# Optimization experiments

Measured on AMD Instinct MI355X. Metric: run time of the kernel, lower is better.

Reference implementation:

```python
import jax, jax.numpy as jnp
import numpy as np

N, E, G, F = 50000, 800000, 64, 128
R_MAX = 5.0
P_CUT = 6.0
NUM_BESSEL = 8


def sph_harm(u):
    # component-normalized real spherical harmonics up to l=3 on unit vectors u [E,3]
    x, y, z = u[:, 0], u[:, 1], u[:, 2]
    one = jnp.ones_like(x)
    s3, s5, s15 = np.sqrt(3.0), np.sqrt(5.0), np.sqrt(15.0)
    c1, c2, c3 = np.sqrt(35.0 / 8.0), np.sqrt(105.0), np.sqrt(21.0 / 8.0)
    c4, c5 = np.sqrt(7.0) / 2.0, np.sqrt(105.0) / 2.0
    x2, y2, z2 = x * x, y * y, z * z
    comps = [
        one,
        s3 * x, s3 * y, s3 * z,
        s15 * x * y, s15 * y * z, 0.5 * s5 * (3.0 * z2 - 1.0), s15 * x * z, 0.5 * s15 * (x2 - y2),
        c1 * y * (3.0 * x2 - y2), c2 * x * y * z, c3 * y * (5.0 * z2 - 1.0),
        c4 * z * (5.0 * z2 - 3.0), c3 * x * (5.0 * z2 - 1.0), c5 * z * (x2 - y2),
        c1 * x * (x2 - 3.0 * y2),
    ]
    return jnp.stack(comps, axis=-1)  # [E,16]


def radial_embedding(r):
    # Bessel basis with polynomial cutoff envelope; r [E]
    n = jnp.arange(1, NUM_BESSEL + 1, dtype=r.dtype)
    bessel = np.sqrt(2.0 / R_MAX) * jnp.sin(n * jnp.pi * r[:, None] / R_MAX) / r[:, None]
    u = r / R_MAX
    p = P_CUT
    env = (1.0 - (p + 1.0) * (p + 2.0) / 2.0 * u ** p
           + p * (p + 2.0) * u ** (p + 1.0)
           - p * (p + 1.0) / 2.0 * u ** (p + 2.0))
    env = env * (r < R_MAX).astype(r.dtype)
    return bessel * env[:, None]  # [E,8]


def setup_inputs() -> dict:
    key = jax.random.key(0)
    ks = jax.random.split(key, 12)
    return {
        "positions": jax.random.normal(ks[0], (N, 3), dtype=jnp.float32),
        "node_attrs": jax.random.uniform(ks[1], (N, 10), dtype=jnp.float32),
        "shifts": jnp.zeros((E, 3), dtype=jnp.float32),
        "edge_index": jax.random.randint(ks[2], (2, E), 0, N),
        "batch": jnp.sort(jax.random.randint(ks[3], (N,), 0, G)),
        "num_graphs": G,
        "W_emb": 0.1 * jax.random.normal(ks[4], (10, F), dtype=jnp.float32),
        "atomic_energies_t": jax.random.normal(ks[5], (10,), dtype=jnp.float32),
        "W_r": 0.1 * jax.random.normal(ks[6], (2, NUM_BESSEL, F), dtype=jnp.float32),
        "w_sh": 0.1 * jax.random.normal(ks[7], (2, 16), dtype=jnp.float32),
        "W_out": 0.1 * jax.random.normal(ks[8], (2, F, F), dtype=jnp.float32),
        "W_skip": 0.1 * jax.random.normal(ks[9], (2, 10, F), dtype=jnp.float32),
        "w_read": 0.1 * jax.random.normal(ks[10], (2, F), dtype=jnp.float32),
    }


def reference(positions, node_attrs, shifts, edge_index, batch, num_graphs,
              W_emb, atomic_energies_t, W_r, w_sh, W_out, W_skip, w_read):
    snd, rcv = edge_index[0], edge_index[1]

    def energy_fn(pos):
        vec = pos[rcv] - pos[snd] + shifts                      # [E,3] edge gather
        r = jnp.sqrt(jnp.sum(vec * vec, axis=-1) + 1e-12)       # [E]
        Y = sph_harm(vec / r[:, None])                          # [E,16]
        eb = radial_embedding(r)                                # [E,8]
        h = node_attrs @ W_emb                                  # [N,F] node embedding
        e0 = jax.ops.segment_sum(node_attrs @ atomic_energies_t, batch, num_segments=num_graphs)
        energy = e0
        for i in range(W_r.shape[0]):                           # interaction layers
            R = eb @ W_r[i]                                     # [E,F] radial weights
            s = Y @ w_sh[i]                                     # [E] angular weight
            m = h[snd] * R * s[:, None]                         # [E,F] messages
            agg = jax.ops.segment_sum(m, rcv, num_segments=pos.shape[0])  # [N,F]
            h = agg @ W_out[i] + node_attrs @ W_skip[i]
            node_e = h @ w_read[i]                              # [N] readout
            energy = energy + jax.ops.segment_sum(node_e, batch, num_segments=num_graphs)
        return energy                                           # [G]

    energy = energy_fn(positions)
    forces = -jax.grad(lambda p: energy_fn(p).sum())(positions)
    return energy, forces
```

## Files before the change

### kernel.cpp

```cpp
#include <hip/hip_runtime.h>

#define NN 50000
#define EE 800000
#define GG 64
#define FF 128
#define NBES 8
#define RECW 8
#define RMAXF 5.0f
#define PI_F 3.14159265358979323846f
#define NB ((NN + 255) / 256)

#define S3  1.7320508075688772f
#define S5  2.23606797749979f
#define S15 3.872983346207417f
#define C1c 2.091650066335189f
#define C2c 10.246950765959598f
#define C3c 1.62018517460196f
#define C4c 1.3228756555322954f
#define C5c 5.123475382979799f
#define CCB 0.6324555320336759f

__device__ __forceinline__ float shc_s(float x, float y, float z, const float* __restrict__ w) {
    float x2 = x * x, y2 = y * y, z2 = z * z;
    return w[0]
        + w[1] * (S3 * x) + w[2] * (S3 * y) + w[3] * (S3 * z)
        + w[4] * (S15 * x * y) + w[5] * (S15 * y * z) + w[6] * (0.5f * S5 * (3.f * z2 - 1.f))
        + w[7] * (S15 * x * z) + w[8] * (0.5f * S15 * (x2 - y2))
        + w[9] * (C1c * y * (3.f * x2 - y2)) + w[10] * (C2c * x * y * z)
        + w[11] * (C3c * y * (5.f * z2 - 1.f)) + w[12] * (C4c * z * (5.f * z2 - 3.f))
        + w[13] * (C3c * x * (5.f * z2 - 1.f)) + w[14] * (C5c * z * (x2 - y2))
        + w[15] * (C1c * x * (x2 - 3.f * y2));
}

__device__ __forceinline__ void shc_grad(float x, float y, float z, const float* __restrict__ w,
                                         float& gx, float& gy, float& gz) {
    float x2 = x * x, y2 = y * y, z2 = z * z;
    gx = w[1] * S3 + w[4] * (S15 * y) + w[7] * (S15 * z) + w[8] * (S15 * x)
       + w[9] * (6.f * C1c * x * y) + w[10] * (C2c * y * z) + w[13] * (C3c * (5.f * z2 - 1.f))
       + w[14] * (2.f * C5c * x * z) + w[15] * (3.f * C1c * (x2 - y2));
    gy = w[2] * S3 + w[4] * (S15 * x) + w[5] * (S15 * z) - w[8] * (S15 * y)
       + w[9] * (3.f * C1c * (x2 - y2)) + w[10] * (C2c * x * z) + w[11] * (C3c * (5.f * z2 - 1.f))
       - w[14] * (2.f * C5c * y * z) - w[15] * (6.f * C1c * x * y);
    gz = w[3] * S3 + w[5] * (S15 * y) + w[6] * (3.f * S5 * z) + w[7] * (S15 * x)
       + w[10] * (C2c * x * y) + w[11] * (10.f * C3c * y * z) + w[12] * (C4c * (15.f * z2 - 3.f))
       + w[13] * (10.f * C3c * x * z) + w[14] * (C5c * (x2 - y2));
}


__global__ __launch_bounds__(256) void count_kernel(const int* __restrict__ ei,
                                                    int* __restrict__ cnt,
                                                    int* __restrict__ rank_r,
                                                    int* __restrict__ rank_s) {
    int e = blockIdx.x * 256 + threadIdx.x;
    if (e >= EE) return;
    rank_r[e] = atomicAdd(&cnt[ei[EE + e]], 1);
    rank_s[e] = atomicAdd(&cnt[NN + ei[e]], 1);
}

__global__ __launch_bounds__(256) void scan_partial(const int* __restrict__ cnt,
                                                    int* __restrict__ parts) {
    __shared__ int wsum[4];
    int b = blockIdx.x;
    int half = b / NB;
    int cb = b - half * NB;
    int i = cb * 256 + threadIdx.x;
    int v = (i < NN) ? cnt[(size_t)half * NN + i] : 0;
    int x = v;
#pragma unroll
    for (int o = 32; o > 0; o >>= 1) x += __shfl_xor(x, o);
    int lane = threadIdx.x & 63, wid = threadIdx.x >> 6;
    if (lane == 0) wsum[wid] = x;
    __syncthreads();
    if (threadIdx.x == 0) parts[b] = wsum[0] + wsum[1] + wsum[2] + wsum[3];
}

__global__ __launch_bounds__(256) void scan_parts(int* __restrict__ parts,
                                                  int* __restrict__ off) {
    __shared__ int wsum[4];
    __shared__ int carry_s;
    int lane = threadIdx.x & 63, wid = threadIdx.x >> 6;
    for (int h = 0; h < 2; h++) {
        if (threadIdx.x == 0) carry_s = 0;
        __syncthreads();
        for (int base = 0; base < NB; base += 256) {
            int i = base + threadIdx.x;
            int v = (i < NB) ? parts[h * NB + i] : 0;
            int x = v;
#pragma unroll
            for (int d = 1; d < 64; d <<= 1) {
                int y = __shfl_up(x, d);
                if (lane >= d) x += y;
            }
            if (lane == 63) wsum[wid] = x;
            __syncthreads();
            int pre = 0;
#pragma unroll
            for (int w = 0; w < 4; w++) if (w < wid) pre += wsum[w];
            int total = wsum[0] + wsum[1] + wsum[2] + wsum[3];
            int carry = carry_s;
            if (i < NB) parts[h * NB + i] = carry + pre + x - v;
            __syncthreads();
            if (threadIdx.x == 0) carry_s = carry + total;
            __syncthreads();
        }
        if (threadIdx.x == 0) off[(size_t)h * (NN + 1) + NN] = carry_s;
        __syncthreads();
    }
}

__global__ __launch_bounds__(256) void scan_apply(const int* __restrict__ cnt,
                                                  const int* __restrict__ parts,
                                                  int* __restrict__ off) {
    __shared__ int wsum[4];
    int b = blockIdx.x;
    int half = b / NB;
    int cb = b - half * NB;
    int i = cb * 256 + threadIdx.x;
    int v = (i < NN) ? cnt[(size_t)half * NN + i] : 0;
    int lane = threadIdx.x & 63, wid = threadIdx.x >> 6;
    int x = v;
#pragma unroll
    for (int d = 1; d < 64; d <<= 1) {
        int y = __shfl_up(x, d);
        if (lane >= d) x += y;
    }
    if (lane == 63) wsum[wid] = x;
    __syncthreads();
    int pre = 0;
#pragma unroll
    for (int w = 0; w < 4; w++) if (w < wid) pre += wsum[w];
    if (i < NN) off[(size_t)half * (NN + 1) + i] = parts[b] + pre + x - v;
}

__global__ __launch_bounds__(256) void fill_kernel(const int* __restrict__ ei,
                                                   const int* __restrict__ off,
                                                   const int* __restrict__ rank_r,
                                                   const int* __restrict__ rank_s,
                                                   int* __restrict__ jr,
                                                   int* __restrict__ js,
                                                   int* __restrict__ psl_j) {
    int e = blockIdx.x * 256 + threadIdx.x;
    if (e >= EE) return;
    int snd = ei[e], rcv = ei[EE + e];
    int sr = off[rcv] + rank_r[e];
    int ss = off[(NN + 1) + snd] + rank_s[e];
    jr[e] = sr;
    js[e] = ss;
    psl_j[ss] = sr;
}


__global__ __launch_bounds__(256) void edge_geom(const float* __restrict__ pos,
                                                 const float* __restrict__ shifts,
                                                 const int* __restrict__ ei,
                                                 const float* __restrict__ wsh,
                                                 const int* __restrict__ jr,
                                                 const int* __restrict__ js,
                                                 float* __restrict__ rec,
                                                 float* __restrict__ ebs0,
                                                 float* __restrict__ ebs1) {
    int e = blockIdx.x * 256 + threadIdx.x;
    if (e >= EE) return;
    int snd = ei[e];
    int rcv = ei[EE + e];
    float vx = pos[rcv * 3 + 0] - pos[snd * 3 + 0] + shifts[e * 3 + 0];
    float vy = pos[rcv * 3 + 1] - pos[snd * 3 + 1] + shifts[e * 3 + 1];
    float vz = pos[rcv * 3 + 2] - pos[snd * 3 + 2] + shifts[e * 3 + 2];
    float r2 = vx * vx + vy * vy + vz * vz + 1e-12f;
    float r = sqrtf(r2);
    float inv_r = 1.0f / r;
    float x = vx * inv_r, y = vy * inv_r, z = vz * inv_r;

    float s0 = shc_s(x, y, z, wsh);
    float s1v = shc_s(x, y, z, wsh + 16);

    float* rc = rec + (size_t)jr[e] * RECW;
    *(float4*)&rc[0] = make_float4(x, y, z, inv_r);
    *(float4*)&rc[4] = make_float4(s0, s1v, __int_as_float(snd), __int_as_float(rcv));

    float u = r * (1.0f / RMAXF);
    float th = PI_F * u;
    float s1 = sinf(th), c1 = cosf(th);
    float u2 = u * u, u3 = u2 * u, u6 = u3 * u3, u7 = u6 * u, u8 = u6 * u2;
    float valid = (r < RMAXF) ? 1.f : 0.f;
    float env = (1.f - 28.f * u6 + 48.f * u7 - 21.f * u8) * valid;
    float base = CCB * inv_r * env;
    float ebv[NBES];
    {
        float sk = s1, skm = 0.f;
        float tc = 2.f * c1;
#pragma unroll
        for (int k = 0; k < NBES; k++) {
            ebv[k] = sk * base;
            float sn = tc * sk - skm; skm = sk; sk = sn;
        }
    }
    float* p0p = ebs0 + (size_t)jr[e] * 8;
    *(float4*)&p0p[0] = make_float4(ebv[0] * s0, ebv[1] * s0, ebv[2] * s0, ebv[3] * s0);
    *(float4*)&p0p[4] = make_float4(ebv[4] * s0, ebv[5] * s0, ebv[6] * s0, ebv[7] * s0);
    float* p1p = ebs1 + (size_t)js[e] * 8;
    *(float4*)&p1p[0] = make_float4(ebv[0] * s1v, ebv[1] * s1v, ebv[2] * s1v, ebv[3] * s1v);
    *(float4*)&p1p[4] = make_float4(ebv[4] * s1v, ebv[5] * s1v, ebv[6] * s1v, ebv[7] * s1v);
}


__global__ __launch_bounds__(256) void e1_csr(const float* __restrict__ ebs1,
                                              const int* __restrict__ off_snd,
                                              float* __restrict__ E1) {
    int gid = blockIdx.x * 256 + threadIdx.x;
    int n = gid >> 3;
    int k_l = gid & 7;
    if (n >= NN) return;
    int beg = off_snd[n], end = off_snd[n + 1];
    float acc = 0.f;
    for (int s = beg; s < end; s++) acc += ebs1[(size_t)s * 8 + k_l];
    E1[(size_t)n * 8 + k_l] = acc;
}


__global__ __launch_bounds__(128) void a1_kernel(const float* __restrict__ Wout1,
                                                 const float* __restrict__ wread1,
                                                 const float* __restrict__ Wskip1,
                                                 const float* __restrict__ ae,
                                                 float* __restrict__ a1,
                                                 float* __restrict__ askip) {
    int f = threadIdx.x;
    float s = 0.f;
    for (int k = 0; k < FF; k++) s += Wout1[f * FF + k] * wread1[k];
    a1[f] = s;
    if (f < 10) {
        float t = 0.f;
        for (int k = 0; k < FF; k++) t += Wskip1[f * FF + k] * wread1[k];
        askip[f] = t + ae[f];
    }
}

__global__ __launch_bounds__(128) void cd_kernel(const float* __restrict__ Wout0,
                                                 const float* __restrict__ wread0,
                                                 const float* __restrict__ a1,
                                                 const float* __restrict__ Wr1,
                                                 float* __restrict__ c0,
                                                 float* __restrict__ D) {
    int fp = threadIdx.x;
    float c = 0.f;
    float d[NBES];
#pragma unroll
    for (int k = 0; k < NBES; k++) d[k] = 0.f;
    for (int f = 0; f < FF; f++) {
        float w = Wout0[fp * FF + f];
        c += wread0[f] * w;
        float aw = a1[f] * w;
#pragma unroll
        for (int k = 0; k < NBES; k++) d[k] += aw * Wr1[k * FF + f];
    }
    c0[fp] = c;
#pragma unroll
    for (int k = 0; k < NBES; k++) D[k * FF + fp] = d[k];
}

__global__ __launch_bounds__(256) void gw_kernel(const float* __restrict__ W_emb,
                                                 const float* __restrict__ Wr0,
                                                 const float* __restrict__ Wout0,
                                                 float* __restrict__ GW) {
    int idx = blockIdx.x * 256 + threadIdx.x;
    if (idx >= 80 * FF) return;
    int fp = idx & 127;
    int p = idx >> 7;
    int a = p >> 3, k = p & 7;
    float s = 0.f;
    for (int f = 0; f < FF; f++)
        s += W_emb[a * FF + f] * Wr0[k * FF + f] * Wout0[f * FF + fp];
    GW[p * FF + fp] = s;
}

__global__ __launch_bounds__(256) void tmc_kernel(const float* __restrict__ D,
                                                  const float* __restrict__ c0,
                                                  const float* __restrict__ W_emb,
                                                  const float* __restrict__ Wr0,
                                                  float* __restrict__ T,
                                                  float* __restrict__ Mc) {
    for (int i = threadIdx.x; i < 720; i += 256) {
        if (i < 640) {
            int kp = i / 80;
            int p0 = i - kp * 80;
            int k = p0 / 10, a = p0 - k * 10;
            float s = 0.f;
            for (int f = 0; f < FF; f++)
                s += D[kp * FF + f] * W_emb[a * FF + f] * Wr0[k * FF + f];
            T[i] = s;
        } else {
            int p0 = i - 640;
            int k = p0 / 10, a = p0 - k * 10;
            float s = 0.f;
            for (int f = 0; f < FF; f++)
                s += c0[f] * W_emb[a * FF + f] * Wr0[k * FF + f];
            Mc[p0] = s;
        }
    }
}


#define P0_BLOCKS 2048
__global__ __launch_bounds__(256) void p0_kernel(const float* __restrict__ rec,
                                                 const float* __restrict__ ebs0,
                                                 const int* __restrict__ off,
                                                 const float* __restrict__ attrs,
                                                 float* __restrict__ P0) {
    int wv = (blockIdx.x * 256 + threadIdx.x) >> 6;
    int lane = threadIdx.x & 63;
    int nwaves = P0_BLOCKS * 4;
    int jsub = lane >> 3;
    int k_l = lane & 7;

    for (int n = wv; n < NN; n += nwaves) {
        int beg = off[n], end = off[n + 1];
        float acc[10];
#pragma unroll
        for (int a = 0; a < 10; a++) acc[a] = 0.f;
        for (int i = beg; i < end; i += 8) {
            int j = i + jsub;
            bool v = (j < end);
            int jc = v ? j : beg;
            float es = ebs0[(size_t)jc * 8 + k_l];
            if (!v) es = 0.f;
            int snd = __float_as_int(rec[(size_t)jc * RECW + 6]);
            const float* at = attrs + (size_t)snd * 10;
#pragma unroll
            for (int a = 0; a < 10; a++) acc[a] += at[a] * es;
        }
#pragma unroll
        for (int a = 0; a < 10; a++) {
            acc[a] += __shfl_xor(acc[a], 8);
            acc[a] += __shfl_xor(acc[a], 16);
            acc[a] += __shfl_xor(acc[a], 32);
        }
        if (jsub == 0) {
#pragma unroll
            for (int a = 0; a < 10; a++)
                P0[(size_t)n * 80 + a * 8 + k_l] = acc[a];
        }
    }
}


#define GEMM_BLOCKS 512
__global__ __launch_bounds__(256, 2) void h1_gemm(const float* __restrict__ P0,
                                                  const float* __restrict__ GW,
                                                  const float* __restrict__ attrs,
                                                  const float* __restrict__ Wskip,
                                                  const float* __restrict__ wread,
                                                  float* __restrict__ h1,
                                                  float* __restrict__ node_e) {
    __shared__ float sb[80][FF];
    __shared__ float sa[32][80];
    int t = threadIdx.x;
#pragma unroll
    for (int j = 0; j < 10; j++) {
        int flat4 = j * 256 + t;
        int row = flat4 >> 5;
        int col = (flat4 & 31) * 4;
        *(float4*)&sb[row][col] = *(const float4*)&GW[row * FF + col];
    }

    int g = t >> 5;
    int f0 = (t & 31) * 4;
    const int NTILES = (NN + 31) / 32;

    for (int tile = blockIdx.x; tile < NTILES; tile += GEMM_BLOCKS) {
        __syncthreads();
#pragma unroll
        for (int j = 0; j < 3; j++) {
            int flat4 = j * 256 + t;
            if (flat4 < 640) {
                int row = flat4 / 20;
                int col = (flat4 - row * 20) * 4;
                int n = tile * 32 + row;
                float4 v = make_float4(0.f, 0.f, 0.f, 0.f);
                if (n < NN) v = *(const float4*)&P0[(size_t)n * 80 + col];
                *(float4*)&sa[row][col] = v;
            }
        }
        __syncthreads();

        float acc[4][4];
#pragma unroll
        for (int i = 0; i < 4; i++)
#pragma unroll
            for (int j = 0; j < 4; j++) acc[i][j] = 0.f;

        for (int kk = 0; kk < 80; kk += 4) {
            float4 bv0 = *(const float4*)&sb[kk + 0][f0];
            float4 bv1 = *(const float4*)&sb[kk + 1][f0];
            float4 bv2 = *(const float4*)&sb[kk + 2][f0];
            float4 bv3 = *(const float4*)&sb[kk + 3][f0];
#pragma unroll
            for (int ni = 0; ni < 4; ni++) {
                float4 av = *(const float4*)&sa[g * 4 + ni][kk];
                acc[ni][0] += av.x * bv0.x + av.y * bv1.x + av.z * bv2.x + av.w * bv3.x;
                acc[ni][1] += av.x * bv0.y + av.y * bv1.y + av.z * bv2.y + av.w * bv3.y;
                acc[ni][2] += av.x * bv0.z + av.y * bv1.z + av.z * bv2.z + av.w * bv3.z;
                acc[ni][3] += av.x * bv0.w + av.y * bv1.w + av.z * bv2.w + av.w * bv3.w;
            }
        }

#pragma unroll
        for (int ni = 0; ni < 4; ni++) {
            int n = tile * 32 + g * 4 + ni;
            bool valid = (n < NN);
#pragma unroll
            for (int a = 0; a < 10; a++) {
                float att = valid ? attrs[n * 10 + a] : 0.f;
                float4 wk = *(const float4*)&Wskip[a * FF + f0];
                acc[ni][0] += att * wk.x;
                acc[ni][1] += att * wk.y;
                acc[ni][2] += att * wk.z;
                acc[ni][3] += att * wk.w;
            }
            if (valid) {
                float4 out;
                out.x = acc[ni][0]; out.y = acc[ni][1];
                out.z = acc[ni][2]; out.w = acc[ni][3];
                *(float4*)&h1[(size_t)n * FF + f0] = out;
            }
            float4 wv = *(const float4*)&wread[f0];
            float p = acc[ni][0] * wv.x + acc[ni][1] * wv.y
                    + acc[ni][2] * wv.z + acc[ni][3] * wv.w;
#pragma unroll
            for (int o = 16; o > 0; o >>= 1) p += __shfl_xor(p, o);
            if (valid && (t & 31) == 0) node_e[n] = p;
        }
    }
}


__global__ __launch_bounds__(256) void t1_kernel(const float* __restrict__ h1,
                                                 const float* __restrict__ a1,
                                                 const float* __restrict__ Wr1,
                                                 float* __restrict__ t1) {
    int w = threadIdx.x >> 6;
    int lane = threadIdx.x & 63;
    int n = blockIdx.x * 4 + w;
    if (n >= NN) return;
    int f0 = lane, f1 = lane + 64;
    float v0 = a1[f0] * h1[(size_t)n * FF + f0];
    float v1 = a1[f1] * h1[(size_t)n * FF + f1];
    float p[NBES];
#pragma unroll
    for (int k = 0; k < NBES; k++)
        p[k] = v0 * Wr1[k * FF + f0] + v1 * Wr1[k * FF + f1];
#pragma unroll
    for (int o = 32; o > 0; o >>= 1) {
#pragma unroll
        for (int k = 0; k < NBES; k++) p[k] += __shfl_xor(p[k], o);
    }
    if (lane == 0) {
        *(float4*)&t1[(size_t)n * 8]     = make_float4(p[0], p[1], p[2], p[3]);
        *(float4*)&t1[(size_t)n * 8 + 4] = make_float4(p[4], p[5], p[6], p[7]);
    }
}


__global__ __launch_bounds__(256) void m_kernel(const float* __restrict__ E1,
                                                const float* __restrict__ T,
                                                const float* __restrict__ Mc,
                                                float* __restrict__ M) {
    __shared__ float sT[720];
    int t = threadIdx.x;
    for (int i = t; i < 720; i += 256) sT[i] = (i < 640) ? T[i] : Mc[i - 640];
    __syncthreads();
    int n = blockIdx.x * 256 + t;
    if (n >= NN) return;
    float4 ea = *(const float4*)&E1[(size_t)n * 8];
    float4 eb = *(const float4*)&E1[(size_t)n * 8 + 4];
    float e1v[8] = {ea.x, ea.y, ea.z, ea.w, eb.x, eb.y, eb.z, eb.w};
#pragma unroll
    for (int c = 0; c < 20; c++) {
        float4 m = *(const float4*)&sT[640 + c * 4];
#pragma unroll
        for (int kp = 0; kp < 8; kp++) {
            float4 tv = *(const float4*)&sT[kp * 80 + c * 4];
            m.x += e1v[kp] * tv.x;
            m.y += e1v[kp] * tv.y;
            m.z += e1v[kp] * tv.z;
            m.w += e1v[kp] * tv.w;
        }
        *(float4*)&M[(size_t)n * 80 + c * 4] = m;
    }
}


#define EP_BLOCKS 512
__global__ __launch_bounds__(256) void edge_pass(const float* __restrict__ rec,
                                                 const float* __restrict__ t1,
                                                 const float* __restrict__ M,
                                                 const float* __restrict__ attrs,
                                                 const int* __restrict__ batch,
                                                 const float* __restrict__ wsh,
                                                 float4* __restrict__ gvp,
                                                 float* __restrict__ energy) {
    __shared__ float eacc[GG];
    int t = threadIdx.x;
    int lane = t & 63;
    if (t < GG) eacc[t] = 0.f;
    __syncthreads();

    for (int j0 = blockIdx.x * 256; j0 < EE; j0 += EP_BLOCKS * 256) {
        int j = j0 + t;
        bool act = (j < EE);
        int jc = act ? j : 0;
        const float* rc = rec + (size_t)jc * RECW;
        float4 q0 = *(const float4*)&rc[0];
        float4 q1 = *(const float4*)&rc[4];
        float x = q0.x, y = q0.y, z = q0.z, ivr = q0.w;
        float s0 = q1.x, s1v = q1.y;
        int snd = __float_as_int(q1.z);
        int rcv = __float_as_int(q1.w);

        float r = 1.0f / ivr;
        float u = r * (1.0f / RMAXF);
        float th = PI_F * u;
        float s1 = sinf(th), c1 = cosf(th);
        float u2 = u * u, u3 = u2 * u, u5 = u2 * u3, u6 = u3 * u3, u7 = u6 * u, u8 = u6 * u2;
        float valid = (r < RMAXF) ? 1.f : 0.f;
        float env = (1.f - 28.f * u6 + 48.f * u7 - 21.f * u8) * valid;
        float denv = (-168.f * u5 + 336.f * u6 - 168.f * u7) * (1.0f / RMAXF) * valid;
        float eb[NBES], db[NBES];
        {
            float sk = s1, skm = 0.f, ck = c1, ckm = 1.f;
            float tc = 2.f * c1;
#pragma unroll
            for (int k = 1; k <= NBES; k++) {
                float b = CCB * sk * ivr;
                eb[k - 1] = b * env;
                db[k - 1] = CCB * (((float)k * PI_F * (1.0f / RMAXF)) * ck * ivr
                                   - sk * ivr * ivr) * env
                            + b * denv;
                float sn = tc * sk - skm; skm = sk; sk = sn;
                float cn = tc * ck - ckm; ckm = ck; ck = cn;
            }
        }

        float4 ta = *(const float4*)&t1[(size_t)snd * 8];
        float4 tb = *(const float4*)&t1[(size_t)snd * 8 + 4];
        float tg[8] = {ta.x, ta.y, ta.z, ta.w, tb.x, tb.y, tb.z, tb.w};
        float dsp1 = 0.f, drp1 = 0.f;
#pragma unroll
        for (int k = 0; k < 8; k++) {
            dsp1 += eb[k] * tg[k];
            drp1 += db[k] * tg[k];
        }

        float at[10];
#pragma unroll
        for (int i = 0; i < 5; i++) {
            float2 v = *(const float2*)&attrs[snd * 10 + 2 * i];
            at[2 * i] = v.x; at[2 * i + 1] = v.y;
        }
        const float* Mr = M + (size_t)rcv * 80;
        float dsp0 = 0.f, drp0 = 0.f;
#pragma unroll
        for (int k = 0; k < 8; k++) {
            float t0 = 0.f;
#pragma unroll
            for (int a = 0; a < 10; a++) t0 += at[a] * Mr[k * 10 + a];
            dsp0 += eb[k] * t0;
            drp0 += db[k] * t0;
        }

        float el = act ? s1v * dsp1 : 0.f;
        int b = act ? batch[rcv] : -1;
        int ub = __builtin_amdgcn_readfirstlane(b);
        if (__all(b == ub)) {
            float es = el;
#pragma unroll
            for (int o = 32; o > 0; o >>= 1) es += __shfl_xor(es, o);
            if (lane == 0 && ub >= 0) atomicAdd(&eacc[ub], es);
        } else {
            if (act) atomicAdd(&eacc[b], el);
        }

        float g0x, g0y, g0z, g1x, g1y, g1z;
        shc_grad(x, y, z, wsh, g0x, g0y, g0z);
        shc_grad(x, y, z, wsh + 16, g1x, g1y, g1z);
        float gux = dsp0 * g0x + dsp1 * g1x;
        float guy = dsp0 * g0y + dsp1 * g1y;
        float guz = dsp0 * g0z + dsp1 * g1z;
        float gr = s0 * drp0 + s1v * drp1;
        float dgu = gux * x + guy * y + guz * z;
        float gvx = gr * x + ivr * (gux - dgu * x);
        float gvy = gr * y + ivr * (guy - dgu * y);
        float gvz = gr * z + ivr * (guz - dgu * z);
        if (act) gvp[j] = make_float4(gvx, gvy, gvz, 0.f);
    }
    __syncthreads();
    if (t < GG && eacc[t] != 0.f) atomicAdd(&energy[t], eacc[t]);
}


__global__ __launch_bounds__(256) void force_gather(const int* __restrict__ off_rcv,
                                                    const int* __restrict__ off_snd,
                                                    const int* __restrict__ psl_j,
                                                    const float4* __restrict__ gvp,
                                                    float* __restrict__ forces) {
    int n = blockIdx.x * 256 + threadIdx.x;
    if (n >= NN) return;
    float fx = 0.f, fy = 0.f, fz = 0.f;
    int beg = off_rcv[n], end = off_rcv[n + 1];
    for (int j = beg; j < end; j++) {
        float4 g = gvp[j];
        fx -= g.x; fy -= g.y; fz -= g.z;
    }
    beg = off_snd[n]; end = off_snd[n + 1];
    for (int s = beg; s < end; s++) {
        float4 g = gvp[psl_j[s]];
        fx += g.x; fy += g.y; fz += g.z;
    }
    forces[n * 3 + 0] = fx;
    forces[n * 3 + 1] = fy;
    forces[n * 3 + 2] = fz;
}


#define EF_BLOCKS 128
__global__ __launch_bounds__(256) void efinal_kernel(const float* __restrict__ node_e,
                                                     const float* __restrict__ attrs,
                                                     const float* __restrict__ askip,
                                                     const int* __restrict__ batch,
                                                     float* __restrict__ energy) {
    __shared__ float eacc[GG];
    int t = threadIdx.x;
    if (t < GG) eacc[t] = 0.f;
    __syncthreads();
    for (int n = blockIdx.x * 256 + t; n < NN; n += EF_BLOCKS * 256) {
        float v = node_e[n];
#pragma unroll
        for (int a = 0; a < 10; a++) v += attrs[n * 10 + a] * askip[a];
        atomicAdd(&eacc[batch[n]], v);
    }
    __syncthreads();
    if (t < GG && eacc[t] != 0.f) atomicAdd(&energy[t], eacc[t]);
}


extern "C" void kernel_launch(void* const* d_in, const int* in_sizes, int n_in,
                              void* d_out, int out_size, void* d_ws, size_t ws_size,
                              hipStream_t stream) {
    const float* pos    = (const float*)d_in[0];
    const float* attrs  = (const float*)d_in[1];
    const float* shifts = (const float*)d_in[2];
    const int*   ei     = (const int*)d_in[3];
    const int*   batch  = (const int*)d_in[4];
    const float* W_emb  = (const float*)d_in[6];
    const float* ae     = (const float*)d_in[7];
    const float* W_r    = (const float*)d_in[8];
    const float* w_sh   = (const float*)d_in[9];
    const float* W_out  = (const float*)d_in[10];
    const float* W_skip = (const float*)d_in[11];
    const float* w_read = (const float*)d_in[12];

    const float* Wr0 = W_r;
    const float* Wr1 = W_r + NBES * FF;
    const float* Wout0 = W_out;
    const float* Wout1 = W_out + FF * FF;

    float* energy = (float*)d_out;
    float* forces = energy + GG;

    float* ws  = (float*)d_ws;
    float* h1  = ws;
    float* P0  = h1 + (size_t)NN * FF;
    float* M   = P0 + (size_t)NN * 80;
    float* E1  = M + (size_t)NN * 80;
    float* t1  = E1 + (size_t)NN * 8;
    float* node_e = t1 + (size_t)NN * 8;
    float* rec = node_e + NN;
    float* ebs0 = rec + (size_t)EE * RECW;
    float* ebs1 = ebs0 + (size_t)EE * 8;
    float4* gvp = (float4*)(ebs1 + (size_t)EE * 8);
    float* a1  = (float*)(gvp + EE);
    float* askip = a1 + FF;
    float* c0  = askip + 16;
    float* D   = c0 + FF;
    float* GW  = D + NBES * FF;
    float* T   = GW + 80 * FF;
    float* Mc  = T + 640;

    int* cnt    = (int*)(Mc + 80);
    int* off    = cnt + 2 * NN;
    int* rank_r = off + 2 * (NN + 1);
    int* rank_s = rank_r + EE;
    int* jr     = rank_s + EE;
    int* js     = jr + EE;
    int* psl_j  = js + EE;
    int* parts  = psl_j + EE;
    const int* off_rcv = off;
    const int* off_snd = off + (NN + 1);

    const int edgeBlocks = (EE + 255) / 256;
    const int nodeBlocks = (NN + 255) / 256;

    hipMemsetAsync(d_out, 0, (size_t)out_size * sizeof(float), stream);
    hipMemsetAsync(cnt, 0, (size_t)2 * NN * sizeof(int), stream);

    count_kernel<<<edgeBlocks, 256, 0, stream>>>(ei, cnt, rank_r, rank_s);
    scan_partial<<<2 * NB, 256, 0, stream>>>(cnt, parts);
    scan_parts<<<1, 256, 0, stream>>>(parts, off);
    scan_apply<<<2 * NB, 256, 0, stream>>>(cnt, parts, off);
    fill_kernel<<<edgeBlocks, 256, 0, stream>>>(ei, off, rank_r, rank_s, jr, js, psl_j);

    a1_kernel<<<1, 128, 0, stream>>>(Wout1, w_read + FF, W_skip + 10 * FF, ae, a1, askip);
    cd_kernel<<<1, 128, 0, stream>>>(Wout0, w_read, a1, Wr1, c0, D);
    gw_kernel<<<40, 256, 0, stream>>>(W_emb, Wr0, Wout0, GW);
    tmc_kernel<<<1, 256, 0, stream>>>(D, c0, W_emb, Wr0, T, Mc);

    edge_geom<<<edgeBlocks, 256, 0, stream>>>(pos, shifts, ei, w_sh, jr, js,
                                              rec, ebs0, ebs1);

    e1_csr<<<(NN * 8 + 255) / 256, 256, 0, stream>>>(ebs1, off_snd, E1);

    p0_kernel<<<P0_BLOCKS, 256, 0, stream>>>(rec, ebs0, off_rcv, attrs, P0);
    h1_gemm<<<GEMM_BLOCKS, 256, 0, stream>>>(P0, GW, attrs, W_skip, w_read, h1, node_e);
    t1_kernel<<<(NN + 3) / 4, 256, 0, stream>>>(h1, a1, Wr1, t1);
    m_kernel<<<nodeBlocks, 256, 0, stream>>>(E1, T, Mc, M);

    edge_pass<<<EP_BLOCKS, 256, 0, stream>>>(rec, t1, M, attrs, batch, w_sh, gvp, energy);

    force_gather<<<nodeBlocks, 256, 0, stream>>>(off_rcv, off_snd, psl_j, gvp, forces);

    efinal_kernel<<<EF_BLOCKS, 256, 0, stream>>>(node_e, attrs, askip, batch, energy);
}
```

Measured before the change: 352.7 us.

## Recompute layer-0 Bessel features in p0 and pad atomic counters

The per-edge layer-0 radial×angular buffer (ebs0) is no longer written by edge_geom. p0_kernel instead recomputes the Bessel and envelope values from the stored inverse distance and s0 in the edge record, trading 32 bytes per edge of write plus read traffic for extra sin and polynomial math. Separately, the node degree counters are padded to a stride of 8 ints so that atomics on different nodes fall on separate cache lines. This reduces contention but multiplies the memset size and makes the scan reads strided.

```diff
diff --git a/kernel.cpp b/kernel.cpp
--- a/kernel.cpp
+++ b/kernel.cpp
@@ -9,6 +9,7 @@
 #define RMAXF 5.0f
 #define PI_F 3.14159265358979323846f
 #define NB ((NN + 255) / 256)
+#define CSTR 8
 
 #define S3  1.7320508075688772f
 #define S5  2.23606797749979f
@@ -53,8 +54,8 @@
                                                     int* __restrict__ rank_s) {
     int e = blockIdx.x * 256 + threadIdx.x;
     if (e >= EE) return;
-    rank_r[e] = atomicAdd(&cnt[ei[EE + e]], 1);
-    rank_s[e] = atomicAdd(&cnt[NN + ei[e]], 1);
+    rank_r[e] = atomicAdd(&cnt[(size_t)ei[EE + e] * CSTR], 1);
+    rank_s[e] = atomicAdd(&cnt[(size_t)(NN + ei[e]) * CSTR], 1);
 }
 
 __global__ __launch_bounds__(256) void scan_partial(const int* __restrict__ cnt,
@@ -64,7 +65,7 @@
     int half = b / NB;
     int cb = b - half * NB;
     int i = cb * 256 + threadIdx.x;
-    int v = (i < NN) ? cnt[(size_t)half * NN + i] : 0;
+    int v = (i < NN) ? cnt[(size_t)(half * NN + i) * CSTR] : 0;
     int x = v;
 #pragma unroll
     for (int o = 32; o > 0; o >>= 1) x += __shfl_xor(x, o);
@@ -116,7 +117,7 @@
     int half = b / NB;
     int cb = b - half * NB;
     int i = cb * 256 + threadIdx.x;
-    int v = (i < NN) ? cnt[(size_t)half * NN + i] : 0;
+    int v = (i < NN) ? cnt[(size_t)(half * NN + i) * CSTR] : 0;
     int lane = threadIdx.x & 63, wid = threadIdx.x >> 6;
     int x = v;
 #pragma unroll
@@ -157,7 +158,6 @@
                                                  const int* __restrict__ jr,
                                                  const int* __restrict__ js,
                                                  float* __restrict__ rec,
-                                                 float* __restrict__ ebs0,
                                                  float* __restrict__ ebs1) {
     int e = blockIdx.x * 256 + threadIdx.x;
     if (e >= EE) return;
@@ -184,7 +184,7 @@
     float u2 = u * u, u3 = u2 * u, u6 = u3 * u3, u7 = u6 * u, u8 = u6 * u2;
     float valid = (r < RMAXF) ? 1.f : 0.f;
     float env = (1.f - 28.f * u6 + 48.f * u7 - 21.f * u8) * valid;
-    float base = CCB * inv_r * env;
+    float base = CCB * inv_r * env * s1v;
     float ebv[NBES];
     {
         float sk = s1, skm = 0.f;
@@ -195,12 +195,9 @@
             float sn = tc * sk - skm; skm = sk; sk = sn;
         }
     }
-    float* p0p = ebs0 + (size_t)jr[e] * 8;
-    *(float4*)&p0p[0] = make_float4(ebv[0] * s0, ebv[1] * s0, ebv[2] * s0, ebv[3] * s0);
-    *(float4*)&p0p[4] = make_float4(ebv[4] * s0, ebv[5] * s0, ebv[6] * s0, ebv[7] * s0);
     float* p1p = ebs1 + (size_t)js[e] * 8;
-    *(float4*)&p1p[0] = make_float4(ebv[0] * s1v, ebv[1] * s1v, ebv[2] * s1v, ebv[3] * s1v);
-    *(float4*)&p1p[4] = make_float4(ebv[4] * s1v, ebv[5] * s1v, ebv[6] * s1v, ebv[7] * s1v);
+    *(float4*)&p1p[0] = make_float4(ebv[0], ebv[1], ebv[2], ebv[3]);
+    *(float4*)&p1p[4] = make_float4(ebv[4], ebv[5], ebv[6], ebv[7]);
 }
 
 
@@ -302,7 +299,6 @@
 
 #define P0_BLOCKS 2048
 __global__ __launch_bounds__(256) void p0_kernel(const float* __restrict__ rec,
-                                                 const float* __restrict__ ebs0,
                                                  const int* __restrict__ off,
                                                  const float* __restrict__ attrs,
                                                  float* __restrict__ P0) {
@@ -311,6 +307,7 @@
     int nwaves = P0_BLOCKS * 4;
     int jsub = lane >> 3;
     int k_l = lane & 7;
+    float kf = (float)(k_l + 1);
 
     for (int n = wv; n < NN; n += nwaves) {
         int beg = off[n], end = off[n + 1];
@@ -321,9 +318,17 @@
             int j = i + jsub;
             bool v = (j < end);
             int jc = v ? j : beg;
-            float es = ebs0[(size_t)jc * 8 + k_l];
-            if (!v) es = 0.f;
-            int snd = __float_as_int(rec[(size_t)jc * RECW + 6]);
+            const float* rc = rec + (size_t)jc * RECW;
+            float ivr = rc[3];
+            float s0 = rc[4];
+            int snd = __float_as_int(rc[6]);
+            float r = 1.0f / ivr;
+            float u = r * (1.0f / RMAXF);
+            float th = PI_F * u;
+            float u2 = u * u, u3 = u2 * u, u6 = u3 * u3, u7 = u6 * u, u8 = u6 * u2;
+            float valid = (r < RMAXF && v) ? 1.f : 0.f;
+            float env = (1.f - 28.f * u6 + 48.f * u7 - 21.f * u8) * valid;
+            float es = sinf(kf * th) * (CCB * ivr * env) * s0;
             const float* at = attrs + (size_t)snd * 10;
 #pragma unroll
             for (int a = 0; a < 10; a++) acc[a] += at[a] * es;
@@ -674,8 +679,7 @@
     float* t1  = E1 + (size_t)NN * 8;
     float* node_e = t1 + (size_t)NN * 8;
     float* rec = node_e + NN;
-    float* ebs0 = rec + (size_t)EE * RECW;
-    float* ebs1 = ebs0 + (size_t)EE * 8;
+    float* ebs1 = rec + (size_t)EE * RECW;
     float4* gvp = (float4*)(ebs1 + (size_t)EE * 8);
     float* a1  = (float*)(gvp + EE);
     float* askip = a1 + FF;
@@ -686,7 +690,7 @@
     float* Mc  = T + 640;
 
     int* cnt    = (int*)(Mc + 80);
-    int* off    = cnt + 2 * NN;
+    int* off    = cnt + (size_t)2 * NN * CSTR;
     int* rank_r = off + 2 * (NN + 1);
     int* rank_s = rank_r + EE;
     int* jr     = rank_s + EE;
@@ -700,7 +704,7 @@
     const int nodeBlocks = (NN + 255) / 256;
 
     hipMemsetAsync(d_out, 0, (size_t)out_size * sizeof(float), stream);
-    hipMemsetAsync(cnt, 0, (size_t)2 * NN * sizeof(int), stream);
+    hipMemsetAsync(cnt, 0, (size_t)2 * NN * CSTR * sizeof(int), stream);
 
     count_kernel<<<edgeBlocks, 256, 0, stream>>>(ei, cnt, rank_r, rank_s);
     scan_partial<<<2 * NB, 256, 0, stream>>>(cnt, parts);
@@ -713,12 +717,11 @@
     gw_kernel<<<40, 256, 0, stream>>>(W_emb, Wr0, Wout0, GW);
     tmc_kernel<<<1, 256, 0, stream>>>(D, c0, W_emb, Wr0, T, Mc);
 
-    edge_geom<<<edgeBlocks, 256, 0, stream>>>(pos, shifts, ei, w_sh, jr, js,
-                                              rec, ebs0, ebs1);
+    edge_geom<<<edgeBlocks, 256, 0, stream>>>(pos, shifts, ei, w_sh, jr, js, rec, ebs1);
 
     e1_csr<<<(NN * 8 + 255) / 256, 256, 0, stream>>>(ebs1, off_snd, E1);
 
-    p0_kernel<<<P0_BLOCKS, 256, 0, stream>>>(rec, ebs0, off_rcv, attrs, P0);
+    p0_kernel<<<P0_BLOCKS, 256, 0, stream>>>(rec, off_rcv, attrs, P0);
     h1_gemm<<<GEMM_BLOCKS, 256, 0, stream>>>(P0, GW, attrs, W_skip, w_read, h1, node_e);
     t1_kernel<<<(NN + 3) / 4, 256, 0, stream>>>(h1, a1, Wr1, t1);
     m_kernel<<<nodeBlocks, 256, 0, stream>>>(E1, T, Mc, M);
```

New measurement: 336.1 us. -4.7%, faster.
